# Kernel tuning notes

Measured on AMD Instinct MI355X. Metric: run time of the kernel, lower is better.

The kernel has to match this reference:

```python
import jax, jax.numpy as jnp
import numpy as np

B, T_ENC, ENC, DEC, MEL = 32, 1024, 1024, 1024, 80


def setup_inputs() -> dict:
    key = jax.random.key(0)
    ks = jax.random.split(key, 10)
    s = lambda k, shape, sc=1.0: (jax.random.normal(k, shape, dtype=jnp.float32) * sc)
    return {
        "prev_mel_frame": s(ks[0], (B, MEL)),
        "encoder_outputs": s(ks[1], (B, T_ENC, ENC)),
        "h": s(ks[2], (B, DEC)),
        "c": s(ks[3], (B, DEC)),
        # AdditiveAttention learned scale vector (use_scale=True default)
        "attn_scale": s(ks[4], (ENC,), 0.05),
        # LSTMCell params: input dim = MEL + ENC, gates order i, f, c, o (Keras)
        "kernel": s(ks[5], (MEL + ENC, 4 * DEC), 0.02),
        "rec_kernel": s(ks[6], (DEC, 4 * DEC), 0.02),
        "bias": s(ks[7], (4 * DEC,), 0.02),
        # Dense projection to mel
        "proj_w": s(ks[8], (DEC, MEL), 0.02),
        "proj_b": s(ks[9], (MEL,), 0.02),
    }


def reference(prev_mel_frame, encoder_outputs, h, c,
              attn_scale, kernel, rec_kernel, bias, proj_w, proj_b):
    # Additive (Bahdanau) attention: scores[b,t] = sum_d scale_d * tanh(h[b,d] + enc[b,t,d])
    feat = jnp.tanh(h[:, None, :] + encoder_outputs)          # [B, T, D]
    scores = jnp.einsum("btd,d->bt", feat, attn_scale)         # [B, T]
    attn = jax.nn.softmax(scores, axis=-1)
    context = jnp.einsum("bt,btd->bd", attn, encoder_outputs)  # [B, ENC]

    # LSTMCell step on concat([prev_mel, context])
    x = jnp.concatenate([prev_mel_frame, context], axis=-1)    # [B, MEL+ENC]
    z = x @ kernel + h @ rec_kernel + bias                     # [B, 4*DEC]
    i, f, g, o = jnp.split(z, 4, axis=-1)
    i = jax.nn.sigmoid(i)
    f = jax.nn.sigmoid(f)
    o = jax.nn.sigmoid(o)
    c_new = f * c + i * jnp.tanh(g)
    h_new = o * jnp.tanh(c_new)

    mel_frame = h_new @ proj_w + proj_b                        # [B, MEL]
    return mel_frame, h_new, c_new
```

## Files before the change

kernel.cpp:

```cpp
#include <hip/hip_runtime.h>

#define BB 32
#define TT 1024
#define ENCD 1024
#define DECD 1024
#define MELD 80
#define KTOT (MELD + ENCD + DECD)
#define NZ (4 * DECD)
#define KCH 64
#define KC 34
#define NTT 32

__device__ float g_cp[NTT * BB * ENCD];
__device__ float g_m[NTT * BB];
__device__ float g_s[NTT * BB];
__device__ float g_ctx[BB * ENCD];
__device__ float g_zp[KC * BB * NZ];
__device__ float g_hn[BB * DECD];

__device__ __forceinline__ float tanh_fast(float x) {
    return 1.f - __fdividef(2.f, __expf(2.f * x) + 1.f);
}
__device__ __forceinline__ float sigmoid_fast(float x) {
    return __fdividef(1.f, 1.f + __expf(-x));
}

__global__ __launch_bounds__(256) void k_attn(const float* __restrict__ enc,
                                              const float* __restrict__ hst,
                                              const float* __restrict__ scale) {
    int b = blockIdx.x, tc = blockIdx.y;
    int w = threadIdx.x >> 6, lane = threadIdx.x & 63;
    const float4* hp = (const float4*)(hst + (size_t)b * DECD);
    const float4* sp = (const float4*)scale;
    float4 hr0 = hp[lane], hr1 = hp[lane + 64], hr2 = hp[lane + 128], hr3 = hp[lane + 192];
    float4 sr0 = sp[lane], sr1 = sp[lane + 64], sr2 = sp[lane + 128], sr3 = sp[lane + 192];

    float m = -1e30f, s = 0.f;
    float4 c0 = {0.f, 0.f, 0.f, 0.f}, c1 = c0, c2 = c0, c3 = c0;

    const float4* ep = (const float4*)(enc + ((size_t)b * TT + tc * 32 + w * 8) * ENCD) + lane;
#pragma unroll 2
    for (int t = 0; t < 8; t++) {
        float4 e0 = ep[t * 256];
        float4 e1 = ep[t * 256 + 64];
        float4 e2 = ep[t * 256 + 128];
        float4 e3 = ep[t * 256 + 192];
        float sc = 0.f;
        sc = fmaf(sr0.x, tanh_fast(hr0.x + e0.x), sc);
        sc = fmaf(sr0.y, tanh_fast(hr0.y + e0.y), sc);
        sc = fmaf(sr0.z, tanh_fast(hr0.z + e0.z), sc);
        sc = fmaf(sr0.w, tanh_fast(hr0.w + e0.w), sc);
        sc = fmaf(sr1.x, tanh_fast(hr1.x + e1.x), sc);
        sc = fmaf(sr1.y, tanh_fast(hr1.y + e1.y), sc);
        sc = fmaf(sr1.z, tanh_fast(hr1.z + e1.z), sc);
        sc = fmaf(sr1.w, tanh_fast(hr1.w + e1.w), sc);
        sc = fmaf(sr2.x, tanh_fast(hr2.x + e2.x), sc);
        sc = fmaf(sr2.y, tanh_fast(hr2.y + e2.y), sc);
        sc = fmaf(sr2.z, tanh_fast(hr2.z + e2.z), sc);
        sc = fmaf(sr2.w, tanh_fast(hr2.w + e2.w), sc);
        sc = fmaf(sr3.x, tanh_fast(hr3.x + e3.x), sc);
        sc = fmaf(sr3.y, tanh_fast(hr3.y + e3.y), sc);
        sc = fmaf(sr3.z, tanh_fast(hr3.z + e3.z), sc);
        sc = fmaf(sr3.w, tanh_fast(hr3.w + e3.w), sc);
#pragma unroll
        for (int off = 32; off; off >>= 1) sc += __shfl_xor(sc, off, 64);
        if (sc > m) {
            float al = __expf(m - sc);
            s = fmaf(s, al, 1.f);
            c0.x = fmaf(c0.x, al, e0.x); c0.y = fmaf(c0.y, al, e0.y);
            c0.z = fmaf(c0.z, al, e0.z); c0.w = fmaf(c0.w, al, e0.w);
            c1.x = fmaf(c1.x, al, e1.x); c1.y = fmaf(c1.y, al, e1.y);
            c1.z = fmaf(c1.z, al, e1.z); c1.w = fmaf(c1.w, al, e1.w);
            c2.x = fmaf(c2.x, al, e2.x); c2.y = fmaf(c2.y, al, e2.y);
            c2.z = fmaf(c2.z, al, e2.z); c2.w = fmaf(c2.w, al, e2.w);
            c3.x = fmaf(c3.x, al, e3.x); c3.y = fmaf(c3.y, al, e3.y);
            c3.z = fmaf(c3.z, al, e3.z); c3.w = fmaf(c3.w, al, e3.w);
            m = sc;
        } else {
            float p = __expf(sc - m);
            s += p;
            c0.x = fmaf(p, e0.x, c0.x); c0.y = fmaf(p, e0.y, c0.y);
            c0.z = fmaf(p, e0.z, c0.z); c0.w = fmaf(p, e0.w, c0.w);
            c1.x = fmaf(p, e1.x, c1.x); c1.y = fmaf(p, e1.y, c1.y);
            c1.z = fmaf(p, e1.z, c1.z); c1.w = fmaf(p, e1.w, c1.w);
            c2.x = fmaf(p, e2.x, c2.x); c2.y = fmaf(p, e2.y, c2.y);
            c2.z = fmaf(p, e2.z, c2.z); c2.w = fmaf(p, e2.w, c2.w);
            c3.x = fmaf(p, e3.x, c3.x); c3.y = fmaf(p, e3.y, c3.y);
            c3.z = fmaf(p, e3.z, c3.z); c3.w = fmaf(p, e3.w, c3.w);
        }
    }

    __shared__ float lm[4], ls[4];
    __shared__ float4 lctx[4][256];
    if (lane == 0) { lm[w] = m; ls[w] = s; }
    __syncthreads();
    float M = fmaxf(fmaxf(lm[0], lm[1]), fmaxf(lm[2], lm[3]));
    float S = ls[0] * __expf(lm[0] - M) + ls[1] * __expf(lm[1] - M) +
              ls[2] * __expf(lm[2] - M) + ls[3] * __expf(lm[3] - M);
    float be = __expf(m - M);
    float4 o;
    o.x = c0.x * be; o.y = c0.y * be; o.z = c0.z * be; o.w = c0.w * be;
    lctx[w][lane] = o;
    o.x = c1.x * be; o.y = c1.y * be; o.z = c1.z * be; o.w = c1.w * be;
    lctx[w][lane + 64] = o;
    o.x = c2.x * be; o.y = c2.y * be; o.z = c2.z * be; o.w = c2.w * be;
    lctx[w][lane + 128] = o;
    o.x = c3.x * be; o.y = c3.y * be; o.z = c3.z * be; o.w = c3.w * be;
    lctx[w][lane + 192] = o;
    __syncthreads();
    int tid = threadIdx.x;
    float4 a0 = lctx[0][tid], a1 = lctx[1][tid], a2 = lctx[2][tid], a3 = lctx[3][tid];
    float4 r;
    r.x = (a0.x + a1.x) + (a2.x + a3.x);
    r.y = (a0.y + a1.y) + (a2.y + a3.y);
    r.z = (a0.z + a1.z) + (a2.z + a3.z);
    r.w = (a0.w + a1.w) + (a2.w + a3.w);
    ((float4*)g_cp)[((size_t)tc * BB + b) * (ENCD / 4) + tid] = r;
    if (tid == 0) { g_m[tc * BB + b] = M; g_s[tc * BB + b] = S; }
}

__global__ __launch_bounds__(256) void k_combine() {
    __shared__ float wgt[NTT];
    int b = blockIdx.x, tid = threadIdx.x;
    float M = -1e30f;
#pragma unroll
    for (int tt = 0; tt < NTT; tt++) M = fmaxf(M, g_m[tt * BB + b]);
    float S = 0.f;
#pragma unroll
    for (int tt = 0; tt < NTT; tt++) S += g_s[tt * BB + b] * __expf(g_m[tt * BB + b] - M);
    if (tid < NTT) wgt[tid] = __expf(g_m[tid * BB + b] - M) * __fdividef(1.f, S);
    __syncthreads();
    const float4* cp = (const float4*)g_cp + (size_t)b * (ENCD / 4) + tid;
    float ax = 0.f, ay = 0.f, az = 0.f, aw = 0.f;
#pragma unroll 8
    for (int tt = 0; tt < NTT; tt++) {
        float4 v = cp[(size_t)tt * (BB * ENCD / 4)];
        float wv = wgt[tt];
        ax = fmaf(wv, v.x, ax); ay = fmaf(wv, v.y, ay);
        az = fmaf(wv, v.z, az); aw = fmaf(wv, v.w, aw);
    }
    float4 r; r.x = ax; r.y = ay; r.z = az; r.w = aw;
    ((float4*)g_ctx)[b * (ENCD / 4) + tid] = r;
}

__global__ __launch_bounds__(256) void k_zmm(const float* __restrict__ pm,
                                             const float* __restrict__ h,
                                             const float* __restrict__ kern,
                                             const float* __restrict__ reck) {
    __shared__ float xs[KCH * 32];
    int jt = blockIdx.x & 15, kc = blockIdx.x >> 4;
    int k0 = kc * KCH;
    int kcount = min(KCH, KTOT - k0);
    int tid = threadIdx.x;
    for (int idx = tid; idx < kcount * 32; idx += 256) {
        int kk = idx >> 5, b = idx & 31;
        int k = k0 + kk;
        float v;
        if (k < MELD)             v = pm[b * MELD + k];
        else if (k < MELD + ENCD) v = g_ctx[b * ENCD + (k - MELD)];
        else                      v = h[b * DECD + (k - MELD - ENCD)];
        xs[idx] = v;
    }
    __syncthreads();
    int j = jt * 256 + tid;
    float acc[32];
#pragma unroll
    for (int b = 0; b < 32; b++) acc[b] = 0.f;
    for (int kk0 = 0; kk0 < kcount; kk0 += 8) {
        float w[8];
#pragma unroll
        for (int i = 0; i < 8; i++) {
            int k = k0 + kk0 + i;
            w[i] = (k < MELD + ENCD) ? kern[(size_t)k * NZ + j]
                                     : reck[(size_t)(k - MELD - ENCD) * NZ + j];
        }
#pragma unroll
        for (int i = 0; i < 8; i++) {
            const float* xr = xs + (kk0 + i) * 32;
#pragma unroll
            for (int b = 0; b < 32; b++) acc[b] = fmaf(xr[b], w[i], acc[b]);
        }
    }
#pragma unroll
    for (int b = 0; b < 32; b++) g_zp[((size_t)kc * BB + b) * NZ + j] = acc[b];
}

__global__ __launch_bounds__(256) void k_gates(const float* __restrict__ bias,
                                               const float* __restrict__ c,
                                               float* __restrict__ out) {
    __shared__ float sacc[4][4][64];
    int b = blockIdx.x >> 4, jq = blockIdx.x & 15;
    int jl = threadIdx.x & 63, grp = threadIdx.x >> 6;
    int j = jq * 64 + jl;
    int kc0 = grp * 9;
    int kc1 = min(kc0 + 9, KC);
    float zi = 0.f, zf = 0.f, zg = 0.f, zo = 0.f;
    for (int kc = kc0; kc < kc1; kc++) {
        const float* zp = g_zp + ((size_t)kc * BB + b) * NZ;
        zi += zp[j];
        zf += zp[1024 + j];
        zg += zp[2048 + j];
        zo += zp[3072 + j];
    }
    sacc[grp][0][jl] = zi; sacc[grp][1][jl] = zf;
    sacc[grp][2][jl] = zg; sacc[grp][3][jl] = zo;
    __syncthreads();
    if (grp == 0) {
        zi = sacc[0][0][jl] + sacc[1][0][jl] + sacc[2][0][jl] + sacc[3][0][jl] + bias[j];
        zf = sacc[0][1][jl] + sacc[1][1][jl] + sacc[2][1][jl] + sacc[3][1][jl] + bias[1024 + j];
        zg = sacc[0][2][jl] + sacc[1][2][jl] + sacc[2][2][jl] + sacc[3][2][jl] + bias[2048 + j];
        zo = sacc[0][3][jl] + sacc[1][3][jl] + sacc[2][3][jl] + sacc[3][3][jl] + bias[3072 + j];
        int idx = b * 1024 + j;
        float cn = sigmoid_fast(zf) * c[idx] + sigmoid_fast(zi) * tanh_fast(zg);
        float hn = sigmoid_fast(zo) * tanh_fast(cn);
        g_hn[idx] = hn;
        out[2560 + idx] = hn;
        out[35328 + idx] = cn;
    }
}

__global__ __launch_bounds__(256) void k_proj(const float* __restrict__ pw,
                                              const float* __restrict__ pb,
                                              float* __restrict__ out) {
    __shared__ float lh[1024];
    __shared__ float pacc[2][MELD];
    int b = blockIdx.x, tid = threadIdx.x;
    for (int i = tid; i < 1024; i += 256) lh[i] = g_hn[b * 1024 + i];
    __syncthreads();
    int m = tid & 127;
    int g = tid >> 7;
    if (m < MELD) {
        float acc = 0.f;
        int d0 = g * 512;
#pragma unroll 8
        for (int d = d0; d < d0 + 512; d++) acc = fmaf(lh[d], pw[d * MELD + m], acc);
        pacc[g][m] = acc;
    }
    __syncthreads();
    if (tid < MELD) out[b * MELD + tid] = pacc[0][tid] + pacc[1][tid] + pb[tid];
}

extern "C" void kernel_launch(void* const* d_in, const int* in_sizes, int n_in,
                              void* d_out, int out_size, void* d_ws, size_t ws_size,
                              hipStream_t stream) {
    const float* pm   = (const float*)d_in[0];
    const float* enc  = (const float*)d_in[1];
    const float* h    = (const float*)d_in[2];
    const float* c    = (const float*)d_in[3];
    const float* asc  = (const float*)d_in[4];
    const float* kern = (const float*)d_in[5];
    const float* reck = (const float*)d_in[6];
    const float* bias = (const float*)d_in[7];
    const float* pw   = (const float*)d_in[8];
    const float* pb   = (const float*)d_in[9];
    float* out = (float*)d_out;

    k_attn   <<<dim3(32, NTT), 256, 0, stream>>>(enc, h, asc);
    k_combine<<<32, 256, 0, stream>>>();
    k_zmm    <<<544, 256, 0, stream>>>(pm, h, kern, reck);
    k_gates  <<<512, 256, 0, stream>>>(bias, c, out);
    k_proj   <<<32, 256, 0, stream>>>(pw, pb, out);
}
```

Baseline: 313.3 us.

## Make attention softmax branchless, widen combine grid, double zmm K-chunk

In the attention kernel, the data-dependent branch in the online softmax becomes a branchless update that always computes both rescale and weight exponentials, and an occupancy hint is added to the launch bounds. The combine kernel is spread over four times as many blocks with scalar loads so more CUs share the context reduction. The GEMM K-chunk doubles, which halves the number of partial-sum slabs written and read by the gates kernel; the gates kernel's per-group chunk ranges are rewritten to match. The trade-offs are extra exp and multiply work per step, and fewer, longer zmm blocks.

```diff
diff --git a/kernel.cpp b/kernel.cpp
--- a/kernel.cpp
+++ b/kernel.cpp
@@ -7,8 +7,8 @@
 #define MELD 80
 #define KTOT (MELD + ENCD + DECD)
 #define NZ (4 * DECD)
-#define KCH 64
-#define KC 34
+#define KCH 128
+#define KC 17
 #define NTT 32
 
 __device__ float g_cp[NTT * BB * ENCD];
@@ -25,9 +25,9 @@
     return __fdividef(1.f, 1.f + __expf(-x));
 }
 
-__global__ __launch_bounds__(256) void k_attn(const float* __restrict__ enc,
-                                              const float* __restrict__ hst,
-                                              const float* __restrict__ scale) {
+__global__ __launch_bounds__(256, 4) void k_attn(const float* __restrict__ enc,
+                                                 const float* __restrict__ hst,
+                                                 const float* __restrict__ scale) {
     int b = blockIdx.x, tc = blockIdx.y;
     int w = threadIdx.x >> 6, lane = threadIdx.x & 63;
     const float4* hp = (const float4*)(hst + (size_t)b * DECD);
@@ -64,30 +64,19 @@
         sc = fmaf(sr3.w, tanh_fast(hr3.w + e3.w), sc);
 #pragma unroll
         for (int off = 32; off; off >>= 1) sc += __shfl_xor(sc, off, 64);
-        if (sc > m) {
-            float al = __expf(m - sc);
-            s = fmaf(s, al, 1.f);
-            c0.x = fmaf(c0.x, al, e0.x); c0.y = fmaf(c0.y, al, e0.y);
-            c0.z = fmaf(c0.z, al, e0.z); c0.w = fmaf(c0.w, al, e0.w);
-            c1.x = fmaf(c1.x, al, e1.x); c1.y = fmaf(c1.y, al, e1.y);
-            c1.z = fmaf(c1.z, al, e1.z); c1.w = fmaf(c1.w, al, e1.w);
-            c2.x = fmaf(c2.x, al, e2.x); c2.y = fmaf(c2.y, al, e2.y);
-            c2.z = fmaf(c2.z, al, e2.z); c2.w = fmaf(c2.w, al, e2.w);
-            c3.x = fmaf(c3.x, al, e3.x); c3.y = fmaf(c3.y, al, e3.y);
-            c3.z = fmaf(c3.z, al, e3.z); c3.w = fmaf(c3.w, al, e3.w);
-            m = sc;
-        } else {
-            float p = __expf(sc - m);
-            s += p;
-            c0.x = fmaf(p, e0.x, c0.x); c0.y = fmaf(p, e0.y, c0.y);
-            c0.z = fmaf(p, e0.z, c0.z); c0.w = fmaf(p, e0.w, c0.w);
-            c1.x = fmaf(p, e1.x, c1.x); c1.y = fmaf(p, e1.y, c1.y);
-            c1.z = fmaf(p, e1.z, c1.z); c1.w = fmaf(p, e1.w, c1.w);
-            c2.x = fmaf(p, e2.x, c2.x); c2.y = fmaf(p, e2.y, c2.y);
-            c2.z = fmaf(p, e2.z, c2.z); c2.w = fmaf(p, e2.w, c2.w);
-            c3.x = fmaf(p, e3.x, c3.x); c3.y = fmaf(p, e3.y, c3.y);
-            c3.z = fmaf(p, e3.z, c3.z); c3.w = fmaf(p, e3.w, c3.w);
-        }
+        float mn = fmaxf(m, sc);
+        float al = __expf(m - mn);
+        float p  = __expf(sc - mn);
+        m = mn;
+        s = fmaf(s, al, p);
+        c0.x = fmaf(p, e0.x, c0.x * al); c0.y = fmaf(p, e0.y, c0.y * al);
+        c0.z = fmaf(p, e0.z, c0.z * al); c0.w = fmaf(p, e0.w, c0.w * al);
+        c1.x = fmaf(p, e1.x, c1.x * al); c1.y = fmaf(p, e1.y, c1.y * al);
+        c1.z = fmaf(p, e1.z, c1.z * al); c1.w = fmaf(p, e1.w, c1.w * al);
+        c2.x = fmaf(p, e2.x, c2.x * al); c2.y = fmaf(p, e2.y, c2.y * al);
+        c2.z = fmaf(p, e2.z, c2.z * al); c2.w = fmaf(p, e2.w, c2.w * al);
+        c3.x = fmaf(p, e3.x, c3.x * al); c3.y = fmaf(p, e3.y, c3.y * al);
+        c3.z = fmaf(p, e3.z, c3.z * al); c3.w = fmaf(p, e3.w, c3.w * al);
     }
 
     __shared__ float lm[4], ls[4];
@@ -121,7 +110,7 @@
 
 __global__ __launch_bounds__(256) void k_combine() {
     __shared__ float wgt[NTT];
-    int b = blockIdx.x, tid = threadIdx.x;
+    int b = blockIdx.x, dq = blockIdx.y, tid = threadIdx.x;
     float M = -1e30f;
 #pragma unroll
     for (int tt = 0; tt < NTT; tt++) M = fmaxf(M, g_m[tt * BB + b]);
@@ -130,17 +119,12 @@
     for (int tt = 0; tt < NTT; tt++) S += g_s[tt * BB + b] * __expf(g_m[tt * BB + b] - M);
     if (tid < NTT) wgt[tid] = __expf(g_m[tid * BB + b] - M) * __fdividef(1.f, S);
     __syncthreads();
-    const float4* cp = (const float4*)g_cp + (size_t)b * (ENCD / 4) + tid;
-    float ax = 0.f, ay = 0.f, az = 0.f, aw = 0.f;
+    int d = dq * 256 + tid;
+    float acc = 0.f;
 #pragma unroll 8
-    for (int tt = 0; tt < NTT; tt++) {
-        float4 v = cp[(size_t)tt * (BB * ENCD / 4)];
-        float wv = wgt[tt];
-        ax = fmaf(wv, v.x, ax); ay = fmaf(wv, v.y, ay);
-        az = fmaf(wv, v.z, az); aw = fmaf(wv, v.w, aw);
-    }
-    float4 r; r.x = ax; r.y = ay; r.z = az; r.w = aw;
-    ((float4*)g_ctx)[b * (ENCD / 4) + tid] = r;
+    for (int tt = 0; tt < NTT; tt++)
+        acc = fmaf(wgt[tt], g_cp[((size_t)tt * BB + b) * ENCD + d], acc);
+    g_ctx[b * ENCD + d] = acc;
 }
 
 __global__ __launch_bounds__(256) void k_zmm(const float* __restrict__ pm,
@@ -192,8 +176,8 @@
     int b = blockIdx.x >> 4, jq = blockIdx.x & 15;
     int jl = threadIdx.x & 63, grp = threadIdx.x >> 6;
     int j = jq * 64 + jl;
-    int kc0 = grp * 9;
-    int kc1 = min(kc0 + 9, KC);
+    int kc0 = (grp == 0) ? 0 : grp * 4 + 1;
+    int kc1 = grp * 4 + 5;
     float zi = 0.f, zf = 0.f, zg = 0.f, zo = 0.f;
     for (int kc = kc0; kc < kc1; kc++) {
         const float* zp = g_zp + ((size_t)kc * BB + b) * NZ;
@@ -256,8 +240,8 @@
     float* out = (float*)d_out;
 
     k_attn   <<<dim3(32, NTT), 256, 0, stream>>>(enc, h, asc);
-    k_combine<<<32, 256, 0, stream>>>();
-    k_zmm    <<<544, 256, 0, stream>>>(pm, h, kern, reck);
+    k_combine<<<dim3(32, 4), 256, 0, stream>>>();
+    k_zmm    <<<272, 256, 0, stream>>>(pm, h, kern, reck);
     k_gates  <<<512, 256, 0, stream>>>(bias, c, out);
     k_proj   <<<32, 256, 0, stream>>>(pw, pb, out);
 }
```

Result: faster. 306.9 us (-2.1%).
